# Kernel optimization log

Measured on AMD Instinct MI355X. Metric: run time of the kernel, lower is better.

Reference implementation:

```python
import jax, jax.numpy as jnp
import numpy as np

LN_EPS = 1e-5


def _ln(h, g, b):
    mu = h.mean(-1, keepdims=True)
    var = ((h - mu) ** 2).mean(-1, keepdims=True)
    return (h - mu) / jnp.sqrt(var + LN_EPS) * g + b


def setup_inputs() -> dict:
    key = jax.random.key(0)
    ks = jax.random.split(key, 12)
    B, T, Cin, C, D, M = 16, 1024, 512, 1024, 256, 1024
    s = 0.02
    inp = {
        "x": jax.random.normal(ks[0], (B, T, Cin), jnp.float32),
        "masks": jnp.ones((B, T), jnp.float32),
        "W1": jax.random.normal(ks[1], (Cin, C), jnp.float32) * s,
        "g1": jnp.ones((C,), jnp.float32), "b1": jnp.zeros((C,), jnp.float32),
        "W2": jax.random.normal(ks[2], (C, C), jnp.float32) * s,
        "g2": jnp.ones((C,), jnp.float32), "b2": jnp.zeros((C,), jnp.float32),
        "W3": jax.random.normal(ks[3], (C, C), jnp.float32) * s,
        "g3": jnp.ones((C,), jnp.float32), "b3": jnp.zeros((C,), jnp.float32),
        "W4": jax.random.normal(ks[4], (C, C), jnp.float32) * s,
        "g4": jnp.ones((C,), jnp.float32), "b4": jnp.zeros((C,), jnp.float32),
        "W5": jax.random.normal(ks[5], (C, D), jnp.float32) * s,
        "b5": jnp.zeros((D,), jnp.float32),
        # Dirichlet(alpha=100) rows, as in the torch init: rows live on the simplex
        "embedding": jax.random.dirichlet(ks[6], jnp.full((D,), 100.0, jnp.float32), (M,)).astype(jnp.float32),
    }
    return inp


def reference(x, masks, W1, g1, b1, W2, g2, b2, W3, g3, b3, W4, g4, b4, W5, b5, embedding):
    h = jax.nn.relu(_ln(x @ W1, g1, b1))
    h = jax.nn.relu(_ln(h @ W2, g2, b2))
    h = jax.nn.relu(_ln(h @ W3, g3, b3))
    h = jax.nn.relu(_ln(h @ W4, g4, b4))
    z = h @ W5 + b5                              # [B, T, D]
    p = jax.nn.log_softmax(z, axis=-1)           # log-prob features

    B, T, D = p.shape
    p_flat = jax.lax.stop_gradient(p.reshape(-1, D))   # x.detach() in torch
    ep = jnp.exp(p_flat)                               # [N, D]
    # KL(exp(p) || e_m) summed over D, for all codes m:
    #   sum_d exp(p)*(p - log(e_m)) = rowsum(exp(p)*p) - exp(p) @ log(E)^T
    div = (ep * p_flat).sum(-1, keepdims=True) - ep @ jnp.log(embedding).T  # [N, M]
    idx = jnp.argmin(div, axis=-1)                     # [N]
    quant = jax.lax.stop_gradient(embedding[idx].reshape(B, T, D))

    # commitment loss: masked KL(exp(p) || quant.detach())
    kl = (jnp.exp(p) * (p - jnp.log(quant))).sum(-1)   # [B, T]
    loss = 0.25 * (kl * masks).mean(0).sum()

    # straight-through estimator
    q = p + jax.lax.stop_gradient(quant - p)
    return z, q, loss
```

## Files before the change

### kernel.cpp

```cpp
#include <hip/hip_runtime.h>
#include <hip/hip_bf16.h>
#include <stdint.h>

typedef __attribute__((ext_vector_type(4))) float f32x4;
typedef __attribute__((ext_vector_type(2))) float f32x2;
typedef __attribute__((ext_vector_type(8))) __bf16 bf16x8;
typedef __attribute__((ext_vector_type(4))) __bf16 bf16x4;

#define LN_EPS 1e-5f

__device__ __forceinline__ void gload_lds16(const void* g, void* l) {
  __builtin_amdgcn_global_load_lds(
      (__attribute__((address_space(1))) void*)(uintptr_t)g,
      (__attribute__((address_space(3))) void*)(uint32_t)(uintptr_t)l,
      16, 0, 0);
}

__device__ __forceinline__ f32x4 mfma16(bf16x8 a, bf16x8 b, f32x4 c) {
  return __builtin_amdgcn_mfma_f32_16x16x32_bf16(a, b, c, 0, 0, 0);
}

__global__ __launch_bounds__(256) void k_cvt_bf16(const float* __restrict__ x,
                                                  __bf16* __restrict__ o) {
  int i = (blockIdx.x * 256 + threadIdx.x) * 8;
  f32x4 a = *(const f32x4*)(x + i);
  f32x4 b = *(const f32x4*)(x + i + 4);
  bf16x8 v;
#pragma unroll
  for (int j = 0; j < 4; ++j) { v[j] = (__bf16)a[j]; v[j + 4] = (__bf16)b[j]; }
  *(bf16x8*)(o + i) = v;
}

__global__ void k_transpose(const float* __restrict__ W, __bf16* __restrict__ Wt,
                            int K, int N) {
  __shared__ float t[32][33];
  int nt = blockIdx.x * 32, kt = blockIdx.y * 32;
  int tx = threadIdx.x, ty = threadIdx.y;
  t[ty][tx] = W[(size_t)(kt + ty) * N + nt + tx];
  __syncthreads();
  Wt[(size_t)(nt + ty) * K + kt + tx] = (__bf16)t[tx][ty];
}

__global__ void k_transpose3(const float* __restrict__ Wa, const float* __restrict__ Wb,
                             const float* __restrict__ Wc, __bf16* __restrict__ Ta,
                             __bf16* __restrict__ Tb, __bf16* __restrict__ Tc) {
  __shared__ float t[32][33];
  const float* W = blockIdx.z == 0 ? Wa : (blockIdx.z == 1 ? Wb : Wc);
  __bf16* T = blockIdx.z == 0 ? Ta : (blockIdx.z == 1 ? Tb : Tc);
  int nt = blockIdx.x * 32, kt = blockIdx.y * 32;
  int tx = threadIdx.x, ty = threadIdx.y;
  t[ty][tx] = W[(size_t)(kt + ty) * 1024 + nt + tx];
  __syncthreads();
  T[(size_t)(nt + ty) * 1024 + kt + tx] = (__bf16)t[tx][ty];
}

__global__ __launch_bounds__(256) void k_logE(const float* __restrict__ e,
                                              __bf16* __restrict__ o) {
  int i = blockIdx.x * 256 + threadIdx.x;
  o[i] = (__bf16)logf(e[i] * 256.0f);
}

__device__ __forceinline__ void gemm256_core(
    const __bf16* __restrict__ A, const __bf16* __restrict__ Bt,
    char* lds, int bm0, int bn0, int K, f32x4 (&acc)[8][4]) {
  const int tid = threadIdx.x;
  const int lane = tid & 63;
  const int wid = tid >> 6;
  const int wm = wid >> 2;
  const int wn = wid & 3;
  const int NT = K >> 6;

  const int slin = tid * 16;
  const int lrow = slin >> 7;
  const int scol = (slin & 127) ^ ((lrow & 7) << 4);
  const char* Ab = (const char*)A;
  const char* Bb = (const char*)Bt;
  const uint32_t rs = (uint32_t)K * 2;

  const int klo = (lane >> 4) * 16;
  const int sw = (lane & 7) << 4;
  const uint32_t kx0 = (uint32_t)(klo ^ sw);
  const uint32_t kx1 = (uint32_t)((64 + klo) ^ sw);
  const uint32_t abase = (uint32_t)(wm * 128 + (lane & 15)) * 128;
  const uint32_t bbase = (uint32_t)(wn * 64 + (lane & 15)) * 128;

#pragma unroll
  for (int i = 0; i < 8; ++i)
#pragma unroll
    for (int j = 0; j < 4; ++j) acc[i][j] = 0.0f;

#define LDSA(buf) (lds + (buf)*32768)
#define LDSB(buf) (lds + 65536 + (buf)*32768)
#define STAGE_A(t, h)                                                              \
  {                                                                                \
    const char* src = Ab + (size_t)(bm0 + (h)*128 + lrow) * rs + ((t) << 7) + scol;\
    char* dst = LDSA((t)&1) + (h)*16384 + slin;                                    \
    gload_lds16(src, dst);                                                         \
    gload_lds16(src + (size_t)64 * rs, dst + 8192);                                \
  }
#define STAGE_B(t, h)                                                              \
  {                                                                                \
    const char* src = Bb + (size_t)(bn0 + (h)*128 + lrow) * rs + ((t) << 7) + scol;\
    char* dst = LDSB((t)&1) + (h)*16384 + slin;                                    \
    gload_lds16(src, dst);                                                         \
    gload_lds16(src + (size_t)64 * rs, dst + 8192);                                \
  }
#define HALF1(Acur, Bcur)                                                          \
  _Pragma("unroll") for (int ni = 0; ni < 4; ++ni) {                               \
    bF[ni][0] = *(const bf16x8*)((Bcur) + bbase + ni * 2048 + kx0);                \
    bF[ni][1] = *(const bf16x8*)((Bcur) + bbase + ni * 2048 + kx1);                \
  }                                                                                \
  {                                                                                \
    bf16x8 aF[4][2];                                                               \
    _Pragma("unroll") for (int mi = 0; mi < 4; ++mi) {                             \
      aF[mi][0] = *(const bf16x8*)((Acur) + abase + mi * 2048 + kx0);              \
      aF[mi][1] = *(const bf16x8*)((Acur) + abase + mi * 2048 + kx1);              \
    }                                                                              \
    __builtin_amdgcn_s_setprio(1);                                                 \
    _Pragma("unroll") for (int mi = 0; mi < 4; ++mi)                               \
        _Pragma("unroll") for (int ni = 0; ni < 4; ++ni) {                         \
          acc[mi][ni] = mfma16(aF[mi][0], bF[ni][0], acc[mi][ni]);                 \
          acc[mi][ni] = mfma16(aF[mi][1], bF[ni][1], acc[mi][ni]);                 \
        }                                                                          \
    __builtin_amdgcn_s_setprio(0);                                                 \
  }
#define HALF2(Acur)                                                                \
  {                                                                                \
    bf16x8 aF[4][2];                                                               \
    _Pragma("unroll") for (int mi = 0; mi < 4; ++mi) {                             \
      aF[mi][0] = *(const bf16x8*)((Acur) + abase + (mi + 4) * 2048 + kx0);        \
      aF[mi][1] = *(const bf16x8*)((Acur) + abase + (mi + 4) * 2048 + kx1);        \
    }                                                                              \
    __builtin_amdgcn_s_setprio(1);                                                 \
    _Pragma("unroll") for (int mi = 0; mi < 4; ++mi)                               \
        _Pragma("unroll") for (int ni = 0; ni < 4; ++ni) {                         \
          acc[mi + 4][ni] = mfma16(aF[mi][0], bF[ni][0], acc[mi + 4][ni]);         \
          acc[mi + 4][ni] = mfma16(aF[mi][1], bF[ni][1], acc[mi + 4][ni]);         \
        }                                                                          \
    __builtin_amdgcn_s_setprio(0);                                                 \
  }

  STAGE_A(0, 0); STAGE_A(0, 1); STAGE_B(0, 0); STAGE_B(0, 1);
  STAGE_B(1, 0); STAGE_B(1, 1);
  asm volatile("s_waitcnt vmcnt(4)");
  __builtin_amdgcn_s_barrier();
  __builtin_amdgcn_sched_barrier(0);

  bf16x8 bF[4][2];
  for (int t = 0; t < NT - 2; ++t) {
    const char* Acur = LDSA(t & 1);
    const char* Bcur = LDSB(t & 1);
    STAGE_A(t + 1, 0); STAGE_A(t + 1, 1);
    HALF1(Acur, Bcur)
    __builtin_amdgcn_s_barrier();
    __builtin_amdgcn_sched_barrier(0);
    STAGE_B(t + 2, 0); STAGE_B(t + 2, 1);
    HALF2(Acur)
    asm volatile("s_waitcnt vmcnt(4)");
    __builtin_amdgcn_s_barrier();
    __builtin_amdgcn_sched_barrier(0);
  }
  {
    const char* Acur = LDSA((NT - 2) & 1);
    const char* Bcur = LDSB((NT - 2) & 1);
    STAGE_A(NT - 1, 0); STAGE_A(NT - 1, 1);
    HALF1(Acur, Bcur)
    __builtin_amdgcn_s_barrier();
    __builtin_amdgcn_sched_barrier(0);
    HALF2(Acur)
    asm volatile("s_waitcnt vmcnt(0)");
    __builtin_amdgcn_s_barrier();
    __builtin_amdgcn_sched_barrier(0);
  }
  {
    const char* Acur = LDSA((NT - 1) & 1);
    const char* Bcur = LDSB((NT - 1) & 1);
    HALF1(Acur, Bcur)
    HALF2(Acur)
  }
#undef STAGE_A
#undef STAGE_B
#undef HALF1
#undef HALF2
#undef LDSA
#undef LDSB
}

__global__ __launch_bounds__(512, 2) void k_gemm256(
    const __bf16* __restrict__ A, const __bf16* __restrict__ Bt,
    __bf16* __restrict__ O, int N, int K) {
  __shared__ char lds[131072];
  const int bm0 = blockIdx.x * 256;
  const int bn0 = blockIdx.y * 256;
  f32x4 acc[8][4];
  gemm256_core(A, Bt, lds, bm0, bn0, K, acc);

  const int lane = threadIdx.x & 63;
  const int wid = threadIdx.x >> 6;
  const int wm = wid >> 2, wn = wid & 3;
  const int r0 = (lane >> 4) * 4;
  const int cc = lane & 15;
#pragma unroll
  for (int mi = 0; mi < 8; ++mi) {
#pragma unroll
    for (int ni = 0; ni < 4; ++ni) {
      int r = bm0 + wm * 128 + mi * 16 + r0;
      int c = bn0 + wn * 64 + ni * 16 + cc;
#pragma unroll
      for (int j = 0; j < 4; ++j)
        O[(size_t)(r + j) * N + c] = (__bf16)acc[mi][ni][j];
    }
  }
}

__global__ __launch_bounds__(512, 2) void k_gemm256_stats(
    const __bf16* __restrict__ A, const __bf16* __restrict__ Bt,
    __bf16* __restrict__ O, f32x2* __restrict__ outPart, int N, int K) {
  __shared__ char lds[131072];
  const int bm0 = blockIdx.x * 256;
  const int bn0 = blockIdx.y * 256;
  f32x4 acc[8][4];
  gemm256_core(A, Bt, lds, bm0, bn0, K, acc);

  const int tid = threadIdx.x;
  const int lane = tid & 63;
  const int wid = tid >> 6;
  const int wm = wid >> 2, wn = wid & 3;
  const int r0 = (lane >> 4) * 4;
  const int cc = lane & 15;

  __builtin_amdgcn_s_barrier();
  float* stp = (float*)lds;
  float* stq = (float*)(lds + 4096);
#pragma unroll
  for (int mi = 0; mi < 8; ++mi) {
#pragma unroll
    for (int j = 0; j < 4; ++j) {
      float s = 0.f, q = 0.f;
#pragma unroll
      for (int ni = 0; ni < 4; ++ni) {
        float v = acc[mi][ni][j];
        s += v; q += v * v;
      }
#pragma unroll
      for (int d = 1; d < 16; d <<= 1) { s += __shfl_xor(s, d); q += __shfl_xor(q, d); }
      if (cc == 0) {
        int rl = wm * 128 + mi * 16 + r0 + j;
        stp[rl * 4 + wn] = s;
        stq[rl * 4 + wn] = q;
      }
    }
  }
  __syncthreads();
  if (tid < 256) {
    float s = stp[tid * 4] + stp[tid * 4 + 1] + stp[tid * 4 + 2] + stp[tid * 4 + 3];
    float q = stq[tid * 4] + stq[tid * 4 + 1] + stq[tid * 4 + 2] + stq[tid * 4 + 3];
    f32x2 pr; pr[0] = s; pr[1] = q;
    outPart[(size_t)(bm0 + tid) * 4 + blockIdx.y] = pr;
  }

#pragma unroll
  for (int mi = 0; mi < 8; ++mi) {
#pragma unroll
    for (int ni = 0; ni < 4; ++ni) {
      int r = bm0 + wm * 128 + mi * 16 + r0;
      int c = bn0 + wn * 64 + ni * 16 + cc;
#pragma unroll
      for (int j = 0; j < 4; ++j)
        O[(size_t)(r + j) * N + c] = (__bf16)acc[mi][ni][j];
    }
  }
}

__global__ __launch_bounds__(512, 2) void k_gemm256_div(
    const __bf16* __restrict__ A, const __bf16* __restrict__ Bt,
    float* __restrict__ part_val, int* __restrict__ part_idx, int N, int K) {
  __shared__ char lds[131072];
  const int bm0 = blockIdx.x * 256;
  const int bn0 = blockIdx.y * 256;
  f32x4 acc[8][4];
  gemm256_core(A, Bt, lds, bm0, bn0, K, acc);

  const int lane = threadIdx.x & 63;
  const int wid = threadIdx.x >> 6;
  const int wm = wid >> 2, wn = wid & 3;
  const int r0 = (lane >> 4) * 4;
  const int cc = lane & 15;
  const int nch = N >> 6;
  const int chunk = (bn0 >> 6) + wn;
#pragma unroll
  for (int mi = 0; mi < 8; ++mi) {
#pragma unroll
    for (int j = 0; j < 4; ++j) {
      float v = acc[mi][0][j];
      int c = cc;
#pragma unroll
      for (int ni = 1; ni < 4; ++ni) {
        float v2 = acc[mi][ni][j];
        int c2 = ni * 16 + cc;
        if (v2 > v) { v = v2; c = c2; }
      }
#pragma unroll
      for (int d = 1; d < 16; d <<= 1) {
        float ov = __shfl_xor(v, d);
        int oc = __shfl_xor(c, d);
        if (ov > v || (ov == v && oc < c)) { v = ov; c = oc; }
      }
      if (cc == 0) {
        int r = bm0 + wm * 128 + mi * 16 + r0 + j;
        part_val[r * nch + chunk] = v;
        part_idx[r * nch + chunk] = bn0 + wn * 64 + c;
      }
    }
  }
}

__global__ __launch_bounds__(256) void k_ln_relu(__bf16* __restrict__ h,
                                                 const float* __restrict__ g,
                                                 const float* __restrict__ b) {
  int lane = threadIdx.x & 63;
  int row = blockIdx.x * 4 + (threadIdx.x >> 6);
  __bf16* rp = h + (size_t)row * 1024;
  bf16x8 v0 = *(const bf16x8*)(rp + lane * 8);
  bf16x8 v1 = *(const bf16x8*)(rp + 512 + lane * 8);
  float f0[8], f1[8];
  float s = 0.f, sq = 0.f;
#pragma unroll
  for (int j = 0; j < 8; ++j) {
    f0[j] = (float)v0[j]; f1[j] = (float)v1[j];
    s += f0[j] + f1[j];
    sq += f0[j] * f0[j] + f1[j] * f1[j];
  }
#pragma unroll
  for (int d = 1; d < 64; d <<= 1) { s += __shfl_xor(s, d); sq += __shfl_xor(sq, d); }
  float mu = s * (1.0f / 1024.0f);
  float var = sq * (1.0f / 1024.0f) - mu * mu;
  float rstd = rsqrtf(var + LN_EPS);
  const f32x4* gv = (const f32x4*)g;
  const f32x4* bv = (const f32x4*)b;
  f32x4 ga0 = gv[lane * 2], ga1 = gv[lane * 2 + 1];
  f32x4 gb0 = gv[128 + lane * 2], gb1 = gv[128 + lane * 2 + 1];
  f32x4 ba0 = bv[lane * 2], ba1 = bv[lane * 2 + 1];
  f32x4 bb0 = bv[128 + lane * 2], bb1 = bv[128 + lane * 2 + 1];
  bf16x8 o0, o1;
#pragma unroll
  for (int j = 0; j < 4; ++j) {
    float t0 = (f0[j] - mu) * rstd * ga0[j] + ba0[j];
    float t1 = (f0[j + 4] - mu) * rstd * ga1[j] + ba1[j];
    float t2 = (f1[j] - mu) * rstd * gb0[j] + bb0[j];
    float t3 = (f1[j + 4] - mu) * rstd * gb1[j] + bb1[j];
    o0[j] = (__bf16)fmaxf(t0, 0.f);
    o0[j + 4] = (__bf16)fmaxf(t1, 0.f);
    o1[j] = (__bf16)fmaxf(t2, 0.f);
    o1[j + 4] = (__bf16)fmaxf(t3, 0.f);
  }
  *(bf16x8*)(rp + lane * 8) = o0;
  *(bf16x8*)(rp + 512 + lane * 8) = o1;
}

__global__ __launch_bounds__(256) void k_gemm_sm(
    const __bf16* __restrict__ A, const __bf16* __restrict__ Bt,
    const float* __restrict__ gw, const float* __restrict__ bw,
    const f32x2* __restrict__ inPart, const float* __restrict__ bias,
    float* __restrict__ z, __bf16* __restrict__ ep, float* __restrict__ sm) {
  const int K = 1024;
  __shared__ char lds[49152];
  const int GBS = 40960;
  char* ldsA = lds;
  char* ldsB = lds + 8192;
  const int tid = threadIdx.x;
  const int lane = tid & 63;
  const int wn = tid >> 6;
  const int bm0 = blockIdx.x * 64;
  const char* Ab = (const char*)A;
  const char* Bb = (const char*)Bt;
  const uint32_t rs = (uint32_t)K * 2;
  const int cc = lane & 15;

  ((f32x4*)(lds + GBS))[tid] = ((const f32x4*)gw)[tid];
  ((f32x4*)(lds + GBS + 4096))[tid] = ((const f32x4*)bw)[tid];

  const int ar0 = tid >> 3;
  float aS[2], cS[2];
#pragma unroll
  for (int i = 0; i < 2; ++i) {
    int r = bm0 + ar0 + i * 32;
    const f32x4* pp = (const f32x4*)(inPart + (size_t)r * 4);
    f32x4 p0 = pp[0], p1 = pp[1];
    float s = p0[0] + p0[2] + p1[0] + p1[2];
    float q = p0[1] + p0[3] + p1[1] + p1[3];
    float mu = s * (1.0f / 1024.0f);
    float var = q * (1.0f / 1024.0f) - mu * mu;
    float rstd = rsqrtf(var + LN_EPS);
    aS[i] = rstd; cS[i] = -mu * rstd;
  }
  const uint32_t acolb = (uint32_t)(tid & 7) * 16;
  const uint32_t awcol = acolb ^ (uint32_t)((ar0 & 7) << 4);

  uint32_t ra[2][4], rb[2][4];
  {
    const int sww = (lane & 7) << 4;
    const int gk = lane & 48;
#pragma unroll
    for (int kk = 0; kk < 2; ++kk) {
#pragma unroll
      for (int i = 0; i < 4; ++i) {
        uint32_t kb = (uint32_t)((kk * 64 + gk) ^ sww);
        ra[kk][i] = (uint32_t)(i * 16 + cc) * 128 + kb;
        rb[kk][i] = (uint32_t)(wn * 64 + i * 16 + cc) * 128 + kb;
      }
    }
  }

  f32x4 acc[4][4];
#pragma unroll
  for (int i = 0; i < 4; ++i)
#pragma unroll
    for (int j = 0; j < 4; ++j) acc[i][j] = 0.0f;

  for (int k0 = 0; k0 < K; k0 += 64) {
    __syncthreads();
    const char* abase_ = Ab + (size_t)(bm0 + ar0) * rs + (size_t)k0 * 2 + acolb;
    bf16x8 a0 = *(const bf16x8*)abase_;
    bf16x8 a1 = *(const bf16x8*)(abase_ + (size_t)32 * rs);
#pragma unroll
    for (int i = 0; i < 8; ++i) {
      int lin = i * 4096 + tid * 16;
      int row = lin >> 7;
      int col = (lin & 127) ^ ((row & 7) << 4);
      gload_lds16(Bb + (size_t)row * rs + k0 * 2 + col, ldsB + lin);
    }
    asm volatile("s_waitcnt vmcnt(8)");
    {
      uint32_t gb_ = GBS + (uint32_t)k0 * 4 + (uint32_t)(tid & 7) * 32;
      f32x4 g0 = *(const f32x4*)(lds + gb_), g1 = *(const f32x4*)(lds + gb_ + 16);
      f32x4 b0 = *(const f32x4*)(lds + gb_ + 4096), b1 = *(const f32x4*)(lds + gb_ + 4112);
      bf16x8 o0, o1;
#pragma unroll
      for (int e = 0; e < 8; ++e) {
        float ge = e < 4 ? g0[e] : g1[e - 4];
        float be = e < 4 ? b0[e] : b1[e - 4];
        float t0 = fmaf(fmaf((float)a0[e], aS[0], cS[0]), ge, be);
        float t1 = fmaf(fmaf((float)a1[e], aS[1], cS[1]), ge, be);
        o0[e] = (__bf16)fmaxf(t0, 0.f);
        o1[e] = (__bf16)fmaxf(t1, 0.f);
      }
      *(bf16x8*)(ldsA + ar0 * 128 + awcol) = o0;
      *(bf16x8*)(ldsA + (ar0 + 32) * 128 + awcol) = o1;
    }
    __syncthreads();
#pragma unroll
    for (int kk = 0; kk < 2; ++kk) {
      bf16x8 af[4], bfv[4];
#pragma unroll
      for (int i = 0; i < 4; ++i) af[i] = *(const bf16x8*)(ldsA + ra[kk][i]);
#pragma unroll
      for (int i = 0; i < 4; ++i) bfv[i] = *(const bf16x8*)(ldsB + rb[kk][i]);
#pragma unroll
      for (int mi = 0; mi < 4; ++mi)
#pragma unroll
        for (int ni = 0; ni < 4; ++ni)
          acc[mi][ni] = mfma16(af[mi], bfv[ni], acc[mi][ni]);
    }
  }

  __syncthreads();
  float* stm = (float*)lds;
  float* sts = (float*)(lds + 1024);
  float* rowm = (float*)(lds + 2048);
  float* rows_ = (float*)(lds + 2304);

  const int r0 = (lane >> 4) * 4;
  float bvv[4];
#pragma unroll
  for (int ni = 0; ni < 4; ++ni) bvv[ni] = bias[wn * 64 + ni * 16 + cc];

#pragma unroll
  for (int mi = 0; mi < 4; ++mi) {
#pragma unroll
    for (int j = 0; j < 4; ++j) {
      float m = -3.4e38f;
#pragma unroll
      for (int ni = 0; ni < 4; ++ni) m = fmaxf(m, acc[mi][ni][j] + bvv[ni]);
#pragma unroll
      for (int d = 1; d < 16; d <<= 1) m = fmaxf(m, __shfl_xor(m, d));
      if (cc == 0) stm[wn * 64 + mi * 16 + r0 + j] = m;
    }
  }
  __syncthreads();
  if (tid < 64) {
    float m = fmaxf(fmaxf(stm[tid], stm[64 + tid]), fmaxf(stm[128 + tid], stm[192 + tid]));
    rowm[tid] = m;
  }
  __syncthreads();
#pragma unroll
  for (int mi = 0; mi < 4; ++mi) {
#pragma unroll
    for (int j = 0; j < 4; ++j) {
      int r = mi * 16 + r0 + j;
      float m = rowm[r];
      float s = 0.f;
#pragma unroll
      for (int ni = 0; ni < 4; ++ni) s += expf(acc[mi][ni][j] + bvv[ni] - m);
#pragma unroll
      for (int d = 1; d < 16; d <<= 1) s += __shfl_xor(s, d);
      if (cc == 0) sts[wn * 64 + r] = s;
    }
  }
  __syncthreads();
  if (tid < 64) {
    float s = sts[tid] + sts[64 + tid] + sts[128 + tid] + sts[192 + tid];
    rows_[tid] = s;
    sm[bm0 + tid] = rowm[tid] + logf(s);
  }
  __syncthreads();
#pragma unroll
  for (int mi = 0; mi < 4; ++mi) {
#pragma unroll
    for (int j = 0; j < 4; ++j) {
      int r = mi * 16 + r0 + j;
      float m = rowm[r];
      float inv = 1.0f / rows_[r];
      float* zp = z + (size_t)(bm0 + r) * 256;
      __bf16* epp = ep + (size_t)(bm0 + r) * 256;
#pragma unroll
      for (int ni = 0; ni < 4; ++ni) {
        int c = wn * 64 + ni * 16 + cc;
        float zz = acc[mi][ni][j] + bvv[ni];
        zp[c] = zz;
        epp[c] = (__bf16)(expf(zz - m) * inv);
      }
    }
  }
}

__global__ __launch_bounds__(256) void k_final(
    const float* __restrict__ part_val, const int* __restrict__ part_idx,
    const float* __restrict__ z, const float* __restrict__ sm,
    const float* __restrict__ emb, const float* __restrict__ masks,
    float* __restrict__ q, float* __restrict__ blockloss) {
  __shared__ float ls[4];
  int lane = threadIdx.x & 63;
  int w = threadIdx.x >> 6;
  int row = blockIdx.x * 4 + w;
  float v = -3.4e38f;
  int c = 0x7fffffff;
  if (lane < 16) { v = part_val[row * 16 + lane]; c = part_idx[row * 16 + lane]; }
#pragma unroll
  for (int d = 1; d < 16; d <<= 1) {
    float ov = __shfl_xor(v, d);
    int oc = __shfl_xor(c, d);
    if (ov > v || (ov == v && oc < c)) { v = ov; c = oc; }
  }
  int code = __shfl(c, 0);
  f32x4 ev = ((const f32x4*)(emb + (size_t)code * 256))[lane];
  ((f32x4*)(q + (size_t)row * 256))[lane] = ev;
  f32x4 zv = ((const f32x4*)(z + (size_t)row * 256))[lane];
  float smr = sm[row];
  float kl = 0.f;
#pragma unroll
  for (int j = 0; j < 4; ++j) {
    float pj = zv[j] - smr;
    kl += expf(pj) * (pj - logf(ev[j]));
  }
#pragma unroll
  for (int d = 1; d < 64; d <<= 1) kl += __shfl_xor(kl, d);
  if (lane == 0) ls[w] = kl * masks[row];
  __syncthreads();
  if (threadIdx.x == 0) blockloss[blockIdx.x] = ls[0] + ls[1] + ls[2] + ls[3];
}

__global__ __launch_bounds__(256) void k_loss_reduce(const float* __restrict__ bl,
                                                     float* __restrict__ out) {
  __shared__ float s[256];
  float a = 0.f;
#pragma unroll
  for (int i = 0; i < 16; ++i) a += bl[threadIdx.x + i * 256];
  s[threadIdx.x] = a;
  __syncthreads();
  for (int st = 128; st > 0; st >>= 1) {
    if (threadIdx.x < st) s[threadIdx.x] += s[threadIdx.x + st];
    __syncthreads();
  }
  if (threadIdx.x == 0) out[0] = s[0] * (0.25f / 16.0f);
}

extern "C" void kernel_launch(void* const* d_in, const int* in_sizes, int n_in,
                              void* d_out, int out_size, void* d_ws, size_t ws_size,
                              hipStream_t stream) {
  const float* x = (const float*)d_in[0];
  const float* masks = (const float*)d_in[1];
  const float* W1 = (const float*)d_in[2];
  const float* g1 = (const float*)d_in[3];
  const float* b1 = (const float*)d_in[4];
  const float* W2 = (const float*)d_in[5];
  const float* g2 = (const float*)d_in[6];
  const float* b2 = (const float*)d_in[7];
  const float* W3 = (const float*)d_in[8];
  const float* g3 = (const float*)d_in[9];
  const float* b3 = (const float*)d_in[10];
  const float* W4 = (const float*)d_in[11];
  const float* g4 = (const float*)d_in[12];
  const float* b4 = (const float*)d_in[13];
  const float* W5 = (const float*)d_in[14];
  const float* b5 = (const float*)d_in[15];
  const float* emb = (const float*)d_in[16];

  const int M = 16384;
  char* ws = (char*)d_ws;
  __bf16* bufA = (__bf16*)(ws);
  __bf16* bufB = (__bf16*)(ws + (32ull << 20));
  __bf16* W1t = (__bf16*)(ws + (64ull << 20));
  __bf16* W2t = (__bf16*)(ws + (65ull << 20));
  __bf16* W3t = (__bf16*)(ws + (67ull << 20));
  __bf16* W4t = (__bf16*)(ws + (69ull << 20));
  __bf16* W5t = (__bf16*)(ws + (71ull << 20));
  __bf16* logE = (__bf16*)(ws + (72ull << 20));
  float* part_val = (float*)(ws + (73ull << 20));
  int* part_idx = (int*)(ws + (74ull << 20));
  float* blockloss = (float*)(ws + (75ull << 20));
  float* sm = (float*)(ws + (76ull << 20));
  f32x2* partB = (f32x2*)(ws + (78ull << 20));
  __bf16* ep = (__bf16*)(ws + (16ull << 20));

  float* z = (float*)d_out;
  float* q = z + (size_t)M * 256;
  float* lossp = z + 2ull * M * 256;

  dim3 tb32(32, 32);
  k_cvt_bf16<<<4096, 256, 0, stream>>>(x, bufB);
  k_transpose<<<dim3(32, 16), tb32, 0, stream>>>(W1, W1t, 512, 1024);
  k_transpose3<<<dim3(32, 32, 3), tb32, 0, stream>>>(W2, W3, W4, W2t, W3t, W4t);
  k_transpose<<<dim3(8, 32), tb32, 0, stream>>>(W5, W5t, 1024, 256);
  k_logE<<<1024, 256, 0, stream>>>(emb, logE);

  k_gemm256<<<dim3(64, 4), 512, 0, stream>>>(bufB, W1t, bufA, 1024, 512);
  k_ln_relu<<<4096, 256, 0, stream>>>(bufA, g1, b1);
  k_gemm256<<<dim3(64, 4), 512, 0, stream>>>(bufA, W2t, bufB, 1024, 1024);
  k_ln_relu<<<4096, 256, 0, stream>>>(bufB, g2, b2);
  k_gemm256<<<dim3(64, 4), 512, 0, stream>>>(bufB, W3t, bufA, 1024, 1024);
  k_ln_relu<<<4096, 256, 0, stream>>>(bufA, g3, b3);
  k_gemm256_stats<<<dim3(64, 4), 512, 0, stream>>>(bufA, W4t, bufB, partB, 1024, 1024);
  k_gemm_sm<<<256, 256, 0, stream>>>(bufB, W5t, g4, b4, partB, b5, z, ep, sm);
  k_gemm256_div<<<dim3(64, 4), 512, 0, stream>>>(ep, logE, part_val, part_idx, 1024, 256);
  k_final<<<4096, 256, 0, stream>>>(part_val, part_idx, z, sm, emb, masks, q, blockloss);
  k_loss_reduce<<<1, 256, 0, stream>>>(blockloss, lossp);
}
```

Baseline: 263.1 us.

## Fuse LayerNorm+ReLU into next GEMM's A-operand load and merge prep kernels

```diff
diff --git a/kernel.cpp b/kernel.cpp
--- a/kernel.cpp
+++ b/kernel.cpp
@@ -20,44 +20,55 @@
   return __builtin_amdgcn_mfma_f32_16x16x32_bf16(a, b, c, 0, 0, 0);
 }
 
-__global__ __launch_bounds__(256) void k_cvt_bf16(const float* __restrict__ x,
-                                                  __bf16* __restrict__ o) {
-  int i = (blockIdx.x * 256 + threadIdx.x) * 8;
-  f32x4 a = *(const f32x4*)(x + i);
-  f32x4 b = *(const f32x4*)(x + i + 4);
-  bf16x8 v;
-#pragma unroll
-  for (int j = 0; j < 4; ++j) { v[j] = (__bf16)a[j]; v[j + 4] = (__bf16)b[j]; }
-  *(bf16x8*)(o + i) = v;
-}
-
-__global__ void k_transpose(const float* __restrict__ W, __bf16* __restrict__ Wt,
-                            int K, int N) {
+__device__ __forceinline__ void transpose256(const float* __restrict__ W,
+                                             __bf16* __restrict__ Wt, int K, int N,
+                                             int nt, int kt, float (*t)[33]) {
+  int tx = threadIdx.x & 31;
+  int ty0 = (threadIdx.x >> 5) * 4;
+#pragma unroll
+  for (int j = 0; j < 4; ++j)
+    t[ty0 + j][tx] = W[(size_t)(kt + ty0 + j) * N + nt + tx];
+  __syncthreads();
+#pragma unroll
+  for (int j = 0; j < 4; ++j)
+    Wt[(size_t)(nt + ty0 + j) * K + kt + tx] = (__bf16)t[tx][ty0 + j];
+}
+
+__global__ __launch_bounds__(256) void k_prep(
+    const float* __restrict__ x, __bf16* __restrict__ xb,
+    const float* __restrict__ W1, __bf16* __restrict__ W1t,
+    const float* __restrict__ W2, __bf16* __restrict__ W2t,
+    const float* __restrict__ W3, __bf16* __restrict__ W3t,
+    const float* __restrict__ W4, __bf16* __restrict__ W4t,
+    const float* __restrict__ W5, __bf16* __restrict__ W5t,
+    const float* __restrict__ emb, __bf16* __restrict__ logE) {
   __shared__ float t[32][33];
-  int nt = blockIdx.x * 32, kt = blockIdx.y * 32;
-  int tx = threadIdx.x, ty = threadIdx.y;
-  t[ty][tx] = W[(size_t)(kt + ty) * N + nt + tx];
-  __syncthreads();
-  Wt[(size_t)(nt + ty) * K + kt + tx] = (__bf16)t[tx][ty];
-}
-
-__global__ void k_transpose3(const float* __restrict__ Wa, const float* __restrict__ Wb,
-                             const float* __restrict__ Wc, __bf16* __restrict__ Ta,
-                             __bf16* __restrict__ Tb, __bf16* __restrict__ Tc) {
-  __shared__ float t[32][33];
-  const float* W = blockIdx.z == 0 ? Wa : (blockIdx.z == 1 ? Wb : Wc);
-  __bf16* T = blockIdx.z == 0 ? Ta : (blockIdx.z == 1 ? Tb : Tc);
-  int nt = blockIdx.x * 32, kt = blockIdx.y * 32;
-  int tx = threadIdx.x, ty = threadIdx.y;
-  t[ty][tx] = W[(size_t)(kt + ty) * 1024 + nt + tx];
-  __syncthreads();
-  T[(size_t)(nt + ty) * 1024 + kt + tx] = (__bf16)t[tx][ty];
-}
-
-__global__ __launch_bounds__(256) void k_logE(const float* __restrict__ e,
-                                              __bf16* __restrict__ o) {
-  int i = blockIdx.x * 256 + threadIdx.x;
-  o[i] = (__bf16)logf(e[i] * 256.0f);
+  const int b = blockIdx.x;
+  if (b < 4096) {
+    int i = (b * 256 + threadIdx.x) * 8;
+    f32x4 a = *(const f32x4*)(x + i);
+    f32x4 c = *(const f32x4*)(x + i + 4);
+    bf16x8 v;
+#pragma unroll
+    for (int j = 0; j < 4; ++j) { v[j] = (__bf16)a[j]; v[j + 4] = (__bf16)c[j]; }
+    *(bf16x8*)(xb + i) = v;
+  } else if (b < 4608) {
+    int b2 = b - 4096;
+    transpose256(W1, W1t, 512, 1024, (b2 & 31) * 32, (b2 >> 5) * 32, t);
+  } else if (b < 7680) {
+    int b3 = b - 4608;
+    int z = b3 >> 10;
+    int b4 = b3 & 1023;
+    const float* W = z == 0 ? W2 : (z == 1 ? W3 : W4);
+    __bf16* T = z == 0 ? W2t : (z == 1 ? W3t : W4t);
+    transpose256(W, T, 1024, 1024, (b4 & 31) * 32, (b4 >> 5) * 32, t);
+  } else if (b < 7936) {
+    int b5 = b - 7680;
+    transpose256(W5, W5t, 1024, 256, (b5 & 7) * 32, (b5 >> 3) * 32, t);
+  } else {
+    int i = (b - 7936) * 256 + threadIdx.x;
+    logE[i] = (__bf16)logf(emb[i] * 256.0f);
+  }
 }
 
 __device__ __forceinline__ void gemm256_core(
@@ -179,37 +190,50 @@
     HALF2(Acur)
   }
 #undef STAGE_A
-#undef STAGE_B
 #undef HALF1
 #undef HALF2
 #undef LDSA
 #undef LDSB
-}
-
-__global__ __launch_bounds__(512, 2) void k_gemm256(
-    const __bf16* __restrict__ A, const __bf16* __restrict__ Bt,
-    __bf16* __restrict__ O, int N, int K) {
-  __shared__ char lds[131072];
-  const int bm0 = blockIdx.x * 256;
-  const int bn0 = blockIdx.y * 256;
-  f32x4 acc[8][4];
-  gemm256_core(A, Bt, lds, bm0, bn0, K, acc);
-
-  const int lane = threadIdx.x & 63;
-  const int wid = threadIdx.x >> 6;
+#undef STAGE_B
+}
+
+__device__ __forceinline__ void stats_epilogue(char* lds, f32x4 (&acc)[8][4],
+                                               f32x2* __restrict__ outPart,
+                                               int bm0) {
+  const int tid = threadIdx.x;
+  const int lane = tid & 63;
+  const int wid = tid >> 6;
   const int wm = wid >> 2, wn = wid & 3;
   const int r0 = (lane >> 4) * 4;
   const int cc = lane & 15;
+  __builtin_amdgcn_s_barrier();
+  float* stp = (float*)lds;
+  float* stq = (float*)(lds + 4096);
 #pragma unroll
   for (int mi = 0; mi < 8; ++mi) {
 #pragma unroll
-    for (int ni = 0; ni < 4; ++ni) {
-      int r = bm0 + wm * 128 + mi * 16 + r0;
-      int c = bn0 + wn * 64 + ni * 16 + cc;
-#pragma unroll
-      for (int j = 0; j < 4; ++j)
-        O[(size_t)(r + j) * N + c] = (__bf16)acc[mi][ni][j];
-    }
+    for (int j = 0; j < 4; ++j) {
+      float s = 0.f, q = 0.f;
+#pragma unroll
+      for (int ni = 0; ni < 4; ++ni) {
+        float v = acc[mi][ni][j];
+        s += v; q += v * v;
+      }
+#pragma unroll
+      for (int d = 1; d < 16; d <<= 1) { s += __shfl_xor(s, d); q += __shfl_xor(q, d); }
+      if (cc == 0) {
+        int rl = wm * 128 + mi * 16 + r0 + j;
+        stp[rl * 4 + wn] = s;
+        stq[rl * 4 + wn] = q;
+      }
+    }
+  }
+  __syncthreads();
+  if (tid < 256) {
+    float s = stp[tid * 4] + stp[tid * 4 + 1] + stp[tid * 4 + 2] + stp[tid * 4 + 3];
+    float q = stq[tid * 4] + stq[tid * 4 + 1] + stq[tid * 4 + 2] + stq[tid * 4 + 3];
+    f32x2 pr; pr[0] = s; pr[1] = q;
+    outPart[(size_t)(bm0 + tid) * 4 + blockIdx.y] = pr;
   }
 }
 
@@ -221,44 +245,12 @@
   const int bn0 = blockIdx.y * 256;
   f32x4 acc[8][4];
   gemm256_core(A, Bt, lds, bm0, bn0, K, acc);
-
-  const int tid = threadIdx.x;
-  const int lane = tid & 63;
-  const int wid = tid >> 6;
+  stats_epilogue(lds, acc, outPart, bm0);
+  const int lane = threadIdx.x & 63;
+  const int wid = threadIdx.x >> 6;
   const int wm = wid >> 2, wn = wid & 3;
   const int r0 = (lane >> 4) * 4;
   const int cc = lane & 15;
-
-  __builtin_amdgcn_s_barrier();
-  float* stp = (float*)lds;
-  float* stq = (float*)(lds + 4096);
-#pragma unroll
-  for (int mi = 0; mi < 8; ++mi) {
-#pragma unroll
-    for (int j = 0; j < 4; ++j) {
-      float s = 0.f, q = 0.f;
-#pragma unroll
-      for (int ni = 0; ni < 4; ++ni) {
-        float v = acc[mi][ni][j];
-        s += v; q += v * v;
-      }
-#pragma unroll
-      for (int d = 1; d < 16; d <<= 1) { s += __shfl_xor(s, d); q += __shfl_xor(q, d); }
-      if (cc == 0) {
-        int rl = wm * 128 + mi * 16 + r0 + j;
-        stp[rl * 4 + wn] = s;
-        stq[rl * 4 + wn] = q;
-      }
-    }
-  }
-  __syncthreads();
-  if (tid < 256) {
-    float s = stp[tid * 4] + stp[tid * 4 + 1] + stp[tid * 4 + 2] + stp[tid * 4 + 3];
-    float q = stq[tid * 4] + stq[tid * 4 + 1] + stq[tid * 4 + 2] + stq[tid * 4 + 3];
-    f32x2 pr; pr[0] = s; pr[1] = q;
-    outPart[(size_t)(bm0 + tid) * 4 + blockIdx.y] = pr;
-  }
-
 #pragma unroll
   for (int mi = 0; mi < 8; ++mi) {
 #pragma unroll
@@ -315,47 +307,193 @@
   }
 }
 
-__global__ __launch_bounds__(256) void k_ln_relu(__bf16* __restrict__ h,
-                                                 const float* __restrict__ g,
-                                                 const float* __restrict__ b) {
-  int lane = threadIdx.x & 63;
-  int row = blockIdx.x * 4 + (threadIdx.x >> 6);
-  __bf16* rp = h + (size_t)row * 1024;
-  bf16x8 v0 = *(const bf16x8*)(rp + lane * 8);
-  bf16x8 v1 = *(const bf16x8*)(rp + 512 + lane * 8);
-  float f0[8], f1[8];
-  float s = 0.f, sq = 0.f;
-#pragma unroll
-  for (int j = 0; j < 8; ++j) {
-    f0[j] = (float)v0[j]; f1[j] = (float)v1[j];
-    s += f0[j] + f1[j];
-    sq += f0[j] * f0[j] + f1[j] * f1[j];
-  }
-#pragma unroll
-  for (int d = 1; d < 64; d <<= 1) { s += __shfl_xor(s, d); sq += __shfl_xor(sq, d); }
-  float mu = s * (1.0f / 1024.0f);
-  float var = sq * (1.0f / 1024.0f) - mu * mu;
-  float rstd = rsqrtf(var + LN_EPS);
-  const f32x4* gv = (const f32x4*)g;
-  const f32x4* bv = (const f32x4*)b;
-  f32x4 ga0 = gv[lane * 2], ga1 = gv[lane * 2 + 1];
-  f32x4 gb0 = gv[128 + lane * 2], gb1 = gv[128 + lane * 2 + 1];
-  f32x4 ba0 = bv[lane * 2], ba1 = bv[lane * 2 + 1];
-  f32x4 bb0 = bv[128 + lane * 2], bb1 = bv[128 + lane * 2 + 1];
-  bf16x8 o0, o1;
-#pragma unroll
-  for (int j = 0; j < 4; ++j) {
-    float t0 = (f0[j] - mu) * rstd * ga0[j] + ba0[j];
-    float t1 = (f0[j + 4] - mu) * rstd * ga1[j] + ba1[j];
-    float t2 = (f1[j] - mu) * rstd * gb0[j] + bb0[j];
-    float t3 = (f1[j + 4] - mu) * rstd * gb1[j] + bb1[j];
-    o0[j] = (__bf16)fmaxf(t0, 0.f);
-    o0[j + 4] = (__bf16)fmaxf(t1, 0.f);
-    o1[j] = (__bf16)fmaxf(t2, 0.f);
-    o1[j + 4] = (__bf16)fmaxf(t3, 0.f);
-  }
-  *(bf16x8*)(rp + lane * 8) = o0;
-  *(bf16x8*)(rp + 512 + lane * 8) = o1;
+__global__ __launch_bounds__(512, 2) void k_gemm256_ln(
+    const __bf16* __restrict__ A, const __bf16* __restrict__ Bt,
+    __bf16* __restrict__ O, const float* __restrict__ gw,
+    const float* __restrict__ bw, const f32x2* __restrict__ inPart,
+    f32x2* __restrict__ outPart, int N, int K) {
+  __shared__ char lds[139264];
+  const int GB = 131072;
+  const int tid = threadIdx.x;
+  const int lane = tid & 63;
+  const int wid = tid >> 6;
+  const int wm = wid >> 2;
+  const int wn = wid & 3;
+  const int bm0 = blockIdx.x * 256;
+  const int bn0 = blockIdx.y * 256;
+  const int NT = K >> 6;
+
+  const int slin = tid * 16;
+  const int lrow = slin >> 7;
+  const int scol = (slin & 127) ^ ((lrow & 7) << 4);
+  const char* Ab = (const char*)A;
+  const char* Bb = (const char*)Bt;
+  const uint32_t rs = (uint32_t)K * 2;
+
+  const int klo = (lane >> 4) * 16;
+  const int sw = (lane & 7) << 4;
+  const uint32_t kx0 = (uint32_t)(klo ^ sw);
+  const uint32_t kx1 = (uint32_t)((64 + klo) ^ sw);
+  const uint32_t abase = (uint32_t)(wm * 128 + (lane & 15)) * 128;
+  const uint32_t bbase = (uint32_t)(wn * 64 + (lane & 15)) * 128;
+
+  const int alrow = tid >> 3;
+  const uint32_t acolb = (uint32_t)(tid & 7) * 16;
+  const uint32_t awcol = acolb ^ (uint32_t)((alrow & 7) << 4);
+  float aS[4], cS[4];
+  bf16x8 ar[4];
+
+  f32x4 acc[8][4];
+#pragma unroll
+  for (int i = 0; i < 8; ++i)
+#pragma unroll
+    for (int j = 0; j < 4; ++j) acc[i][j] = 0.0f;
+
+#define LDSA(buf) (lds + (buf)*32768)
+#define LDSB(buf) (lds + 65536 + (buf)*32768)
+#define STAGE_B(t, h)                                                              \
+  {                                                                                \
+    const char* src = Bb + (size_t)(bn0 + (h)*128 + lrow) * rs + ((t) << 7) + scol;\
+    char* dst = LDSB((t)&1) + (h)*16384 + slin;                                    \
+    gload_lds16(src, dst);                                                         \
+    gload_lds16(src + (size_t)64 * rs, dst + 8192);                                \
+  }
+#define A_ISSUE(t1)                                                               \
+  {                                                                               \
+    const char* base_ = Ab + (size_t)(bm0 + alrow) * rs + ((size_t)(t1) << 7) + acolb; \
+    ar[0] = *(const bf16x8*)(base_);                                              \
+    ar[1] = *(const bf16x8*)(base_ + (size_t)64 * rs);                            \
+    ar[2] = *(const bf16x8*)(base_ + (size_t)128 * rs);                           \
+    ar[3] = *(const bf16x8*)(base_ + (size_t)192 * rs);                           \
+  }
+#define A_WRITE(t1)                                                               \
+  {                                                                               \
+    uint32_t gb_ = GB + (uint32_t)(t1)*256 + (uint32_t)(tid & 7) * 32;            \
+    f32x4 g0 = *(const f32x4*)(lds + gb_), g1 = *(const f32x4*)(lds + gb_ + 16);  \
+    f32x4 b0 = *(const f32x4*)(lds + gb_ + 4096), b1 = *(const f32x4*)(lds + gb_ + 4112); \
+    char* wb_ = LDSA((t1)&1);                                                     \
+    _Pragma("unroll") for (int i = 0; i < 4; ++i) {                               \
+      bf16x8 v = ar[i], o;                                                        \
+      _Pragma("unroll") for (int e = 0; e < 8; ++e) {                             \
+        float xv = (float)v[e];                                                   \
+        float tt = fmaf(xv, aS[i], cS[i]);                                        \
+        float ge = e < 4 ? g0[e] : g1[e - 4];                                     \
+        float be = e < 4 ? b0[e] : b1[e - 4];                                     \
+        tt = fmaf(tt, ge, be);                                                    \
+        o[e] = (__bf16)fmaxf(tt, 0.f);                                            \
+      }                                                                           \
+      *(bf16x8*)(wb_ + (i >> 1) * 16384 + (alrow + (i & 1) * 64) * 128 + awcol) = o; \
+    }                                                                             \
+  }
+
+  if (tid < 256) {
+    ((f32x4*)(lds + GB))[tid] = ((const f32x4*)gw)[tid];
+    ((f32x4*)(lds + GB + 4096))[tid] = ((const f32x4*)bw)[tid];
+  }
+#pragma unroll
+  for (int i = 0; i < 4; ++i) {
+    int r = bm0 + (i >> 1) * 128 + (i & 1) * 64 + alrow;
+    const f32x4* pp = (const f32x4*)(inPart + (size_t)r * 4);
+    f32x4 p0 = pp[0], p1 = pp[1];
+    float s = p0[0] + p0[2] + p1[0] + p1[2];
+    float q = p0[1] + p0[3] + p1[1] + p1[3];
+    float mu = s * (1.0f / 1024.0f);
+    float var = q * (1.0f / 1024.0f) - mu * mu;
+    float rstd = rsqrtf(var + LN_EPS);
+    aS[i] = rstd;
+    cS[i] = -mu * rstd;
+  }
+  __builtin_amdgcn_sched_barrier(0);
+  A_ISSUE(0)
+  STAGE_B(0, 0); STAGE_B(0, 1); STAGE_B(1, 0); STAGE_B(1, 1);
+  __builtin_amdgcn_sched_barrier(0);
+  asm volatile("s_waitcnt lgkmcnt(0)");
+  __builtin_amdgcn_s_barrier();
+  asm volatile("s_waitcnt vmcnt(8)");
+  A_WRITE(0)
+  asm volatile("s_waitcnt vmcnt(4) lgkmcnt(0)");
+  __builtin_amdgcn_s_barrier();
+  __builtin_amdgcn_sched_barrier(0);
+
+  for (int t = 0; t < NT; ++t) {
+    const char* Acur = LDSA(t & 1);
+    const char* Bcur = LDSB(t & 1);
+
+    if (t + 1 < NT) { A_ISSUE(t + 1) }
+    bf16x8 bF[4][2];
+#pragma unroll
+    for (int ni = 0; ni < 4; ++ni) {
+      bF[ni][0] = *(const bf16x8*)(Bcur + bbase + ni * 2048 + kx0);
+      bF[ni][1] = *(const bf16x8*)(Bcur + bbase + ni * 2048 + kx1);
+    }
+    {
+      bf16x8 aF[4][2];
+#pragma unroll
+      for (int mi = 0; mi < 4; ++mi) {
+        aF[mi][0] = *(const bf16x8*)(Acur + abase + mi * 2048 + kx0);
+        aF[mi][1] = *(const bf16x8*)(Acur + abase + mi * 2048 + kx1);
+      }
+      __builtin_amdgcn_s_setprio(1);
+#pragma unroll
+      for (int mi = 0; mi < 4; ++mi)
+#pragma unroll
+        for (int ni = 0; ni < 4; ++ni) {
+          acc[mi][ni] = mfma16(aF[mi][0], bF[ni][0], acc[mi][ni]);
+          acc[mi][ni] = mfma16(aF[mi][1], bF[ni][1], acc[mi][ni]);
+        }
+      __builtin_amdgcn_s_setprio(0);
+    }
+    __builtin_amdgcn_s_barrier();
+    __builtin_amdgcn_sched_barrier(0);
+
+    if (t + 2 < NT) { STAGE_B(t + 2, 0); STAGE_B(t + 2, 1); }
+    {
+      bf16x8 aF[4][2];
+#pragma unroll
+      for (int mi = 0; mi < 4; ++mi) {
+        aF[mi][0] = *(const bf16x8*)(Acur + abase + (mi + 4) * 2048 + kx0);
+        aF[mi][1] = *(const bf16x8*)(Acur + abase + (mi + 4) * 2048 + kx1);
+      }
+      __builtin_amdgcn_s_setprio(1);
+#pragma unroll
+      for (int mi = 0; mi < 4; ++mi)
+#pragma unroll
+        for (int ni = 0; ni < 4; ++ni) {
+          acc[mi + 4][ni] = mfma16(aF[mi][0], bF[ni][0], acc[mi + 4][ni]);
+          acc[mi + 4][ni] = mfma16(aF[mi][1], bF[ni][1], acc[mi + 4][ni]);
+        }
+      __builtin_amdgcn_s_setprio(0);
+    }
+    if (t + 1 < NT) {
+      if (t + 2 < NT) { asm volatile("s_waitcnt vmcnt(4)"); }
+      else            { asm volatile("s_waitcnt vmcnt(0)"); }
+      A_WRITE(t + 1)
+      asm volatile("s_waitcnt lgkmcnt(0)");
+      __builtin_amdgcn_s_barrier();
+      __builtin_amdgcn_sched_barrier(0);
+    }
+  }
+#undef STAGE_B
+#undef A_ISSUE
+#undef A_WRITE
+#undef LDSA
+#undef LDSB
+
+  stats_epilogue(lds, acc, outPart, bm0);
+
+  const int r0 = (lane >> 4) * 4;
+  const int cc = lane & 15;
+#pragma unroll
+  for (int mi = 0; mi < 8; ++mi) {
+#pragma unroll
+    for (int ni = 0; ni < 4; ++ni) {
+      int r = bm0 + wm * 128 + mi * 16 + r0;
+      int c = bn0 + wn * 64 + ni * 16 + cc;
+#pragma unroll
+      for (int j = 0; j < 4; ++j)
+        O[(size_t)(r + j) * N + c] = (__bf16)acc[mi][ni][j];
+    }
+  }
 }
 
 __global__ __launch_bounds__(256) void k_gemm_sm(
@@ -620,6 +758,7 @@
   int* part_idx = (int*)(ws + (74ull << 20));
   float* blockloss = (float*)(ws + (75ull << 20));
   float* sm = (float*)(ws + (76ull << 20));
+  f32x2* partA = (f32x2*)(ws + (77ull << 20));
   f32x2* partB = (f32x2*)(ws + (78ull << 20));
   __bf16* ep = (__bf16*)(ws + (16ull << 20));
 
@@ -627,20 +766,12 @@
   float* q = z + (size_t)M * 256;
   float* lossp = z + 2ull * M * 256;
 
-  dim3 tb32(32, 32);
-  k_cvt_bf16<<<4096, 256, 0, stream>>>(x, bufB);
-  k_transpose<<<dim3(32, 16), tb32, 0, stream>>>(W1, W1t, 512, 1024);
-  k_transpose3<<<dim3(32, 32, 3), tb32, 0, stream>>>(W2, W3, W4, W2t, W3t, W4t);
-  k_transpose<<<dim3(8, 32), tb32, 0, stream>>>(W5, W5t, 1024, 256);
-  k_logE<<<1024, 256, 0, stream>>>(emb, logE);
-
-  k_gemm256<<<dim3(64, 4), 512, 0, stream>>>(bufB, W1t, bufA, 1024, 512);
-  k_ln_relu<<<4096, 256, 0, stream>>>(bufA, g1, b1);
-  k_gemm256<<<dim3(64, 4), 512, 0, stream>>>(bufA, W2t, bufB, 1024, 1024);
-  k_ln_relu<<<4096, 256, 0, stream>>>(bufB, g2, b2);
-  k_gemm256<<<dim3(64, 4), 512, 0, stream>>>(bufB, W3t, bufA, 1024, 1024);
-  k_ln_relu<<<4096, 256, 0, stream>>>(bufA, g3, b3);
-  k_gemm256_stats<<<dim3(64, 4), 512, 0, stream>>>(bufA, W4t, bufB, partB, 1024, 1024);
+  k_prep<<<8960, 256, 0, stream>>>(x, bufB, W1, W1t, W2, W2t, W3, W3t, W4, W4t,
+                                   W5, W5t, emb, logE);
+  k_gemm256_stats<<<dim3(64, 4), 512, 0, stream>>>(bufB, W1t, bufA, partA, 1024, 512);
+  k_gemm256_ln<<<dim3(64, 4), 512, 0, stream>>>(bufA, W2t, bufB, g1, b1, partA, partB, 1024, 1024);
+  k_gemm256_ln<<<dim3(64, 4), 512, 0, stream>>>(bufB, W3t, bufA, g2, b2, partB, partA, 1024, 1024);
+  k_gemm256_ln<<<dim3(64, 4), 512, 0, stream>>>(bufA, W4t, bufB, g3, b3, partA, partB, 1024, 1024);
   k_gemm_sm<<<256, 256, 0, stream>>>(bufB, W5t, g4, b4, partB, b5, z, ep, sm);
   k_gemm256_div<<<dim3(64, 4), 512, 0, stream>>>(ep, logE, part_val, part_idx, 1024, 256);
   k_final<<<4096, 256, 0, stream>>>(part_val, part_idx, z, sm, emb, masks, q, blockloss);
```

After: 252.7 us. 3.9% less time.
